# Performance work log

Hardware: AMD Instinct MI355X
Metric: run time of the kernel (lower is better)

The kernel has to match this reference:

```python
import jax, jax.numpy as jnp
import numpy as np
from jax.ops import segment_sum

N_NODE, N_EDGE, D_IN, D_HID, N_CLS = 50000, 800000, 64, 64, 40


def setup_inputs() -> dict:
    key = jax.random.key(0)
    k1, k2, k3, k4 = jax.random.split(key, 4)
    x = jax.random.normal(k1, (N_NODE, D_IN), dtype=jnp.float32)
    edge_index = jax.random.randint(k2, (2, N_EDGE), 0, N_NODE, dtype=jnp.int64)
    W1 = jax.random.normal(k3, (D_IN, D_HID), dtype=jnp.float32) * (1.0 / np.sqrt(D_IN))
    b1 = jnp.zeros((D_HID,), dtype=jnp.float32)
    W2 = jax.random.normal(k4, (D_HID, N_CLS), dtype=jnp.float32) * (1.0 / np.sqrt(D_HID))
    b2 = jnp.zeros((N_CLS,), dtype=jnp.float32)
    return {"x": x, "edge_index": edge_index, "W1": W1, "b1": b1, "W2": W2, "b2": b2}


def _att_weights(fea, row, col, n):
    # edge-parallel cosine similarity (sklearn cosine_similarity restricted to edges)
    nrm = jnp.sqrt(jnp.sum(fea * fea, axis=1, keepdims=True))
    fn = fea / jnp.maximum(nrm, 1e-12)
    sim = jnp.sum(fn[row] * fn[col], axis=1)                 # [E]
    sim = jnp.where(sim < 0.1, 0.0, sim)                      # threshold
    # L1 row-normalization (sim >= 0 after threshold)
    rs = segment_sum(sim, row, num_segments=n)                # [N]
    sim_n = jnp.where(sim > 0, sim / jnp.maximum(rs[row], 1e-12), 0.0)
    # degree-based self-loop weight lam = 1/(deg+1)
    deg = segment_sum((sim > 0).astype(fea.dtype), row, num_segments=n)
    lam = 1.0 / (deg + 1.0)
    # exp applied only to stored (nonzero) entries; zeroed edges stay 0
    w_edge = jnp.where(sim > 0, jnp.exp(sim_n), 0.0)          # [E]
    w_self = jnp.exp(lam)                                     # [N] self-loop weights
    return w_edge, w_self


def _gcn(h, W, b, row, col, w_edge, w_self, n):
    # symmetric-norm GCN over weighted edges + explicit self loops
    deg = segment_sum(w_edge, row, num_segments=n) + w_self
    dinv = 1.0 / jnp.sqrt(jnp.maximum(deg, 1e-12))
    h = h @ W                                                 # [N, F]
    coef = w_edge * dinv[row] * dinv[col]                     # [E]
    out = segment_sum(coef[:, None] * h[col], row, num_segments=n)
    out = out + (w_self * dinv * dinv)[:, None] * h + b
    return out


def reference(x, edge_index, W1, b1, W2, b2):
    n = x.shape[0]
    row, col = edge_index[0], edge_index[1]
    # layer 1: attention coefs from raw features
    w1e, w1s = _att_weights(x, row, col, n)
    h = jax.nn.relu(_gcn(x, W1, b1, row, col, w1e, w1s, n))
    # layer 2: attention coefs recomputed on hidden features (dropout = eval mode)
    w2e, w2s = _att_weights(h, row, col, n)
    out = _gcn(h, W2, b2, row, col, w2e, w2s, n)
    return jax.nn.log_softmax(out, axis=1)
```

## Files before the change

kernel.cpp:

```cpp
#include <hip/hip_runtime.h>
#include <math.h>


#define ATT_CAP 96
#define EPB     2048
#define RPB     128
#define NBUCK_MAX 512
#define CAPB    4096

__global__ void k_normfn(const float* __restrict__ fea, float* __restrict__ fn, int n)
{
    int gid  = blockIdx.x * blockDim.x + threadIdx.x;
    int wid  = gid >> 6;
    int lane = threadIdx.x & 63;
    if (wid >= n) return;
    float v = fea[(size_t)wid * 64 + lane];
    float s = v * v;
#pragma unroll
    for (int off = 32; off > 0; off >>= 1) s += __shfl_xor(s, off);
    float inv = 1.0f / fmaxf(sqrtf(s), 1e-12f);
    fn[(size_t)wid * 64 + lane] = v * inv;
}

__global__ void k_bhist(const int* __restrict__ row, int* __restrict__ hist,
                        int* __restrict__ btot, int E, int nblkA, int nbuck)
{
    __shared__ int lh[NBUCK_MAX];
    int b = blockIdx.x;
    int ebeg = b * EPB, eend = ebeg + EPB; if (eend > E) eend = E;
    for (int i = threadIdx.x; i < nbuck; i += blockDim.x) lh[i] = 0;
    __syncthreads();
    for (int e = ebeg + threadIdx.x; e < eend; e += blockDim.x)
        atomicAdd(&lh[row[e] >> 7], 1);
    __syncthreads();
    for (int i = threadIdx.x; i < nbuck; i += blockDim.x) {
        int c = lh[i];
        hist[(size_t)i * nblkA + b] = c;
        if (c) atomicAdd(btot + i, c);
    }
}

__global__ void k_bscan(const int* __restrict__ btot, int* __restrict__ bbase, int nbuck)
{
    int lane = threadIdx.x;
    int K = (nbuck + 63) / 64;
    int beg = lane * K;
    int s = 0;
    for (int i = 0; i < K; ++i) { int idx = beg + i; if (idx < nbuck) s += btot[idx]; }
    int incl = s;
#pragma unroll
    for (int off = 1; off < 64; off <<= 1) {
        int v = __shfl_up(incl, off);
        if (lane >= off) incl += v;
    }
    int run = incl - s;
    for (int i = 0; i < K; ++i) {
        int idx = beg + i;
        if (idx < nbuck) { bbase[idx] = run; run += btot[idx]; }
    }
    if (lane == 63) bbase[nbuck] = incl;
}

__global__ void k_mscan(int* __restrict__ hist, const int* __restrict__ bbase,
                        int nbuck, int nblkA)
{
    int wib  = threadIdx.x >> 6;
    int j    = blockIdx.x * 4 + wib;
    int lane = threadIdx.x & 63;
    if (j >= nbuck) return;
    int run = bbase[j];
    size_t base = (size_t)j * nblkA;
    for (int b0 = 0; b0 < nblkA; b0 += 64) {
        int b = b0 + lane;
        int v = (b < nblkA) ? hist[base + b] : 0;
        int incl = v;
#pragma unroll
        for (int off = 1; off < 64; off <<= 1) {
            int t = __shfl_up(incl, off);
            if (lane >= off) incl += t;
        }
        if (b < nblkA) hist[base + b] = run + (incl - v);
        run += __shfl(incl, 63);
    }
}

__global__ void k_bscat(const int* __restrict__ row, const int* __restrict__ col,
                        const int* __restrict__ hist, int* __restrict__ ebuf,
                        int E, int nblkA, int nbuck)
{
    __shared__ int lh[NBUCK_MAX];
    int b = blockIdx.x;
    int ebeg = b * EPB, eend = ebeg + EPB; if (eend > E) eend = E;
    for (int i = threadIdx.x; i < nbuck; i += blockDim.x)
        lh[i] = hist[(size_t)i * nblkA + b];
    __syncthreads();
    for (int e = ebeg + threadIdx.x; e < eend; e += blockDim.x) {
        int r = row[e];
        int j = r >> 7;
        int pos = atomicAdd(&lh[j], 1);
        ebuf[pos] = ((r & (RPB - 1)) << 16) | col[e];
    }
}

__global__ void k_csr(const int* __restrict__ ebuf, const int* __restrict__ bbase,
                      int* __restrict__ rptr, int* __restrict__ col_s, int N, int E)
{
    __shared__ int pk[CAPB];
    __shared__ int lcol[CAPB];
    __shared__ int lcnt[RPB], lexc[RPB], lcur[RPB];
    int j = blockIdx.x;
    int beg = bbase[j], end = bbase[j + 1];
    int m = end - beg; if (m > CAPB) m = CAPB;
    int tid = threadIdx.x;
    for (int i = tid; i < m; i += blockDim.x) pk[i] = ebuf[beg + i];
    if (tid < RPB) lcnt[tid] = 0;
    __syncthreads();
    for (int i = tid; i < m; i += blockDim.x) atomicAdd(&lcnt[pk[i] >> 16], 1);
    __syncthreads();
    if (tid < 64) {
        int a = lcnt[2 * tid], b2 = lcnt[2 * tid + 1];
        int s = a + b2;
        int incl = s;
#pragma unroll
        for (int off = 1; off < 64; off <<= 1) {
            int v = __shfl_up(incl, off);
            if (tid >= off) incl += v;
        }
        int base = incl - s;
        lexc[2 * tid] = base;     lexc[2 * tid + 1] = base + a;
        lcur[2 * tid] = base;     lcur[2 * tid + 1] = base + a;
    }
    __syncthreads();
    for (int i = tid; i < m; i += blockDim.x) {
        int v = pk[i];
        int p = atomicAdd(&lcur[v >> 16], 1);
        lcol[p] = v & 0xFFFF;
    }
    __syncthreads();
    for (int i = tid; i < m; i += blockDim.x) col_s[beg + i] = lcol[i];
    if (tid < RPB) {
        int r = j * RPB + tid;
        if (r < N) rptr[r] = beg + lexc[tid];
    }
    if (j == 0 && tid == 0) rptr[N] = E;
}

__global__ void k_att(const float* __restrict__ fn,
                      const int* __restrict__ rptr, const int* __restrict__ col_s,
                      int* __restrict__ col_live, float* __restrict__ w_live,
                      int* __restrict__ lend, float* __restrict__ dinv,
                      float* __restrict__ selfc, int n)
{
    __shared__ float ssim[4][ATT_CAP];
    __shared__ int   scol[4][ATT_CAP];
    int wib  = threadIdx.x >> 6;
    int wid  = blockIdx.x * 4 + wib;
    int lane = threadIdx.x & 63;
    if (wid >= n) return;
    int sub = lane & 7;
    int grp = lane >> 3;
    int beg = rptr[wid], end = rptr[wid + 1];
    int deg_all = end - beg;

    const float4* frp = (const float4*)(fn + (size_t)wid * 64);
    float4 a0 = frp[sub * 2], a1 = frp[sub * 2 + 1];

    float rs_part = 0.0f;
    int ngrp = (deg_all + 7) >> 3;
    for (int g = 0; g < ngrp; ++g) {
        int li = g * 8 + grp;
        float s = 0.0f; int c = 0;
        bool valid = (li < deg_all);
        if (valid) {
            c = col_s[beg + li];
            const float4* fcp = (const float4*)(fn + (size_t)c * 64);
            float4 b0 = fcp[sub * 2], b1 = fcp[sub * 2 + 1];
            float p = a0.x * b0.x + a0.y * b0.y + a0.z * b0.z + a0.w * b0.w
                    + a1.x * b1.x + a1.y * b1.y + a1.z * b1.z + a1.w * b1.w;
            p += __shfl_xor(p, 1);
            p += __shfl_xor(p, 2);
            p += __shfl_xor(p, 4);
            s = (p < 0.1f) ? 0.0f : p;
        }
        if (sub == 0 && valid) {
            if (li < ATT_CAP) { ssim[wib][li] = s; scol[wib][li] = c; }
            if (s > 0.0f) rs_part += s;
        }
    }
#pragma unroll
    for (int off = 32; off > 0; off >>= 1) rs_part += __shfl_xor(rs_part, off);
    float denom = fmaxf(rs_part, 1e-12f);

    int   nlive = 0;
    float sw_lane = 0.0f;
    for (int base = 0; base < deg_all; base += 64) {
        int li = base + lane;
        bool valid = (li < deg_all);
        float s = 0.0f; int c = 0;
        if (valid) {
            if (li < ATT_CAP) { s = ssim[wib][li]; c = scol[wib][li]; }
            else {
                c = col_s[beg + li];
                const float* fr = fn + (size_t)wid * 64;
                const float* fc = fn + (size_t)c * 64;
                float p = 0.0f;
                for (int k = 0; k < 64; ++k) p += fr[k] * fc[k];
                s = (p < 0.1f) ? 0.0f : p;
            }
        }
        float w = (valid && s > 0.0f) ? expf(s / denom) : 0.0f;
        unsigned long long M = __ballot(w > 0.0f);
        int rank = __popcll(M & ((1ull << lane) - 1ull));
        if (w > 0.0f) {
            col_live[beg + nlive + rank] = c;
            w_live[beg + nlive + rank]   = w;
            sw_lane += w;
        }
        nlive += __popcll(M);
    }
#pragma unroll
    for (int off = 32; off > 0; off >>= 1) sw_lane += __shfl_xor(sw_lane, off);

    if (lane == 0) {
        float wself = expf(1.0f / ((float)nlive + 1.0f));
        float D  = sw_lane + wself;
        float di = rsqrtf(fmaxf(D, 1e-12f));
        lend[wid]  = beg + nlive;
        dinv[wid]  = di;
        selfc[wid] = wself * di * di;
    }
}

template <int F, typename InT, typename OutT>
__global__ void k_gemm(const InT* __restrict__ fea, const float* __restrict__ W,
                       OutT* __restrict__ out, int n)
{
    constexpr int R = 256 / F;
    __shared__ float sW[64 * F];
    __shared__ float sX[R * 64];
    int tid = threadIdx.x;
    for (int i = tid; i < 64 * F; i += 256) sW[i] = W[i];
    int base = blockIdx.x * R;
    for (int i = tid; i < R * 64; i += 256) {
        int rr = base + i / 64;
        sX[i] = (rr < n) ? (float)fea[(size_t)rr * 64 + (i & 63)] : 0.0f;
    }
    __syncthreads();
    int rl = tid / F, j = tid % F;
    if (rl >= R) return;
    int r = base + rl;
    if (r >= n) return;
    float acc = 0.0f;
#pragma unroll
    for (int k = 0; k < 64; ++k) acc = fmaf(sX[rl * 64 + k], sW[k * F + j], acc);
    out[(size_t)r * F + j] = (OutT)acc;
}

template <int F>
__device__ inline float agg_core_live(const _Float16* __restrict__ h,
                                      const float* __restrict__ dinv,
                                      const int* __restrict__ col_live,
                                      const float* __restrict__ w_live,
                                      int beg, int lend_, int lane)
{
    float acc = 0.0f;
    bool active = (F == 64) ? true : (lane < F);
    for (int base = beg; base < lend_; base += 64) {
        int idx = base + lane;
        int cv = 0; float wv = 0.0f;
        if (idx < lend_) { cv = col_live[idx]; wv = w_live[idx]; }
        int cnt = lend_ - base; if (cnt > 64) cnt = 64;
        for (int j = 0; j < cnt; j += 4) {
            int   c0 = __shfl(cv, j);     float w0 = __shfl(wv, j);
            int   c1 = __shfl(cv, j + 1); float w1 = __shfl(wv, j + 1);
            int   c2 = __shfl(cv, j + 2); float w2 = __shfl(wv, j + 2);
            int   c3 = __shfl(cv, j + 3); float w3 = __shfl(wv, j + 3);
            float d0 = dinv[c0], d1 = dinv[c1], d2 = dinv[c2], d3 = dinv[c3];
            float h0 = 0.0f, h1 = 0.0f, h2 = 0.0f, h3 = 0.0f;
            if (active) {
                h0 = (float)h[(size_t)c0 * F + lane];
                h1 = (float)h[(size_t)c1 * F + lane];
                h2 = (float)h[(size_t)c2 * F + lane];
                h3 = (float)h[(size_t)c3 * F + lane];
            }
            acc += w0 * d0 * h0;
            acc += w1 * d1 * h1;
            acc += w2 * d2 * h2;
            acc += w3 * d3 * h3;
        }
    }
    return acc;
}

__global__ void k_agg64(const _Float16* __restrict__ h, const float* __restrict__ w_live,
                        const int* __restrict__ col_live,
                        const float* __restrict__ dinv, const float* __restrict__ selfc,
                        const float* __restrict__ b, const int* __restrict__ row_ptr,
                        const int* __restrict__ lend,
                        _Float16* __restrict__ hrelu16, float* __restrict__ fnh, int n)
{
    int gid  = blockIdx.x * blockDim.x + threadIdx.x;
    int wid  = gid >> 6;
    int lane = threadIdx.x & 63;
    if (wid >= n) return;
    int beg = row_ptr[wid], le = lend[wid];
    float acc = agg_core_live<64>(h, dinv, col_live, w_live, beg, le, lane);
    float hs  = (float)h[(size_t)wid * 64 + lane];
    float v = dinv[wid] * acc + selfc[wid] * hs + b[lane];
    v = fmaxf(v, 0.0f);
    hrelu16[(size_t)wid * 64 + lane] = (_Float16)v;
    float s = v * v;
#pragma unroll
    for (int off = 32; off > 0; off >>= 1) s += __shfl_xor(s, off);
    float inv = 1.0f / fmaxf(sqrtf(s), 1e-12f);
    fnh[(size_t)wid * 64 + lane] = v * inv;
}

__global__ void k_agg40_lsm(const _Float16* __restrict__ h2, const float* __restrict__ w_live,
                            const int* __restrict__ col_live,
                            const float* __restrict__ dinv, const float* __restrict__ selfc,
                            const float* __restrict__ b, const int* __restrict__ row_ptr,
                            const int* __restrict__ lend,
                            float* __restrict__ out, int n)
{
    constexpr int F = 40;
    int gid  = blockIdx.x * blockDim.x + threadIdx.x;
    int wid  = gid >> 6;
    int lane = threadIdx.x & 63;
    if (wid >= n) return;
    int beg = row_ptr[wid], le = lend[wid];
    float acc = agg_core_live<F>(h2, dinv, col_live, w_live, beg, le, lane);
    bool active = (lane < F);
    float v = 0.0f;
    if (active) {
        float hs = (float)h2[(size_t)wid * F + lane];
        v = dinv[wid] * acc + selfc[wid] * hs + b[lane];
    }
    float m = active ? v : -__builtin_inff();
#pragma unroll
    for (int off = 32; off > 0; off >>= 1) m = fmaxf(m, __shfl_xor(m, off));
    float ex = active ? expf(v - m) : 0.0f;
    float s = ex;
#pragma unroll
    for (int off = 32; off > 0; off >>= 1) s += __shfl_xor(s, off);
    if (active) out[(size_t)wid * F + lane] = v - m - logf(s);
}

extern "C" void kernel_launch(void* const* d_in, const int* in_sizes, int n_in,
                              void* d_out, int out_size, void* d_ws, size_t ws_size,
                              hipStream_t stream)
{
    const float* x  = (const float*)d_in[0];
    const int*   ei = (const int*)d_in[1];
    const float* W1 = (const float*)d_in[2];
    const float* b1 = (const float*)d_in[3];
    const float* W2 = (const float*)d_in[4];
    const float* b2 = (const float*)d_in[5];
    float* out = (float*)d_out;

    const int N = in_sizes[0] / 64;
    const int E = in_sizes[1] / 2;
    const int* row = ei;
    const int* col = ei + E;

    const int nblkA = (E + EPB - 1) / EPB;
    const int nbuck = (N + RPB - 1) / RPB;

    char* p = (char*)d_ws;
    auto alloc = [&](size_t bytes) -> char* {
        char* r = p; p += (bytes + 255) & ~(size_t)255; return r;
    };
    float*     fn     = (float*)alloc((size_t)N * 64 * 4);
    float*     dinv   = (float*)alloc((size_t)N * 4);
    float*     selfc  = (float*)alloc((size_t)N * 4);
    _Float16*  h1h    = (_Float16*)alloc((size_t)N * 64 * 2);
    _Float16*  hrelu  = (_Float16*)alloc((size_t)N * 64 * 2);
    _Float16*  h2h    = (_Float16*)alloc((size_t)N * 40 * 2);
    float*     fnh    = (float*)alloc((size_t)N * 64 * 4);
    int*       rptr   = (int*)alloc((size_t)(N + 1) * 4);
    int*       lendv  = (int*)alloc((size_t)N * 4);
    int*       col_s  = (int*)alloc((size_t)E * 4);
    int*       col_lv = (int*)alloc((size_t)E * 4);
    float*     w_lv   = (float*)alloc((size_t)E * 4);
    int*       ebuf   = (int*)alloc((size_t)E * 4);
    int*       hist   = (int*)alloc((size_t)nbuck * nblkA * 4);
    int*       btot   = (int*)alloc((size_t)nbuck * 4);
    int*       bbase  = (int*)alloc((size_t)(nbuck + 1) * 4);

    const int TB = 256;
    int blk_nodeWave = (N * 64 + TB - 1) / TB;
    int blk_node4    = (N + 3) / 4;

    hipMemsetAsync(btot, 0, (size_t)nbuck * 4, stream);

    k_bhist<<<nblkA, TB, 0, stream>>>(row, hist, btot, E, nblkA, nbuck);
    k_bscan<<<1, 64, 0, stream>>>(btot, bbase, nbuck);
    k_mscan<<<(nbuck + 3) / 4, TB, 0, stream>>>(hist, bbase, nbuck, nblkA);
    k_bscat<<<nblkA, TB, 0, stream>>>(row, col, hist, ebuf, E, nblkA, nbuck);
    k_csr<<<nbuck, TB, 0, stream>>>(ebuf, bbase, rptr, col_s, N, E);

    k_normfn<<<blk_nodeWave, TB, 0, stream>>>(x, fn, N);
    k_att<<<blk_node4, TB, 0, stream>>>(fn, rptr, col_s, col_lv, w_lv, lendv,
                                        dinv, selfc, N);
    k_gemm<64, float, _Float16><<<(N + 3) / 4, TB, 0, stream>>>(x, W1, h1h, N);
    k_agg64<<<blk_nodeWave, TB, 0, stream>>>(h1h, w_lv, col_lv, dinv, selfc, b1,
                                             rptr, lendv, hrelu, fnh, N);

    k_att<<<blk_node4, TB, 0, stream>>>(fnh, rptr, col_s, col_lv, w_lv, lendv,
                                        dinv, selfc, N);
    k_gemm<40, _Float16, _Float16><<<(N + 5) / 6, TB, 0, stream>>>(hrelu, W2, h2h, N);
    k_agg40_lsm<<<blk_nodeWave, TB, 0, stream>>>(h2h, w_lv, col_lv, dinv, selfc, b2,
                                                 rptr, lendv, out, N);
}
```

Baseline: 288.8 us.

## Prescale features by dinv, pack col/weight pairs, vectorize edge gather

Measured after the change: 285.5 us. About the same (-1.1%).

```diff
diff --git a/kernel.cpp b/kernel.cpp
--- a/kernel.cpp
+++ b/kernel.cpp
@@ -7,6 +7,8 @@
 #define RPB     128
 #define NBUCK_MAX 512
 #define CAPB    4096
+
+typedef _Float16 half4 __attribute__((ext_vector_type(4)));
 
 __global__ void k_normfn(const float* __restrict__ fea, float* __restrict__ fn, int n)
 {
@@ -147,9 +149,8 @@
 
 __global__ void k_att(const float* __restrict__ fn,
                       const int* __restrict__ rptr, const int* __restrict__ col_s,
-                      int* __restrict__ col_live, float* __restrict__ w_live,
-                      int* __restrict__ lend, float* __restrict__ dinv,
-                      float* __restrict__ selfc, int n)
+                      int2* __restrict__ cw, int* __restrict__ lend,
+                      float* __restrict__ dinv, float* __restrict__ selfc, int n)
 {
     __shared__ float ssim[4][ATT_CAP];
     __shared__ int   scol[4][ATT_CAP];
@@ -212,8 +213,8 @@
         unsigned long long M = __ballot(w > 0.0f);
         int rank = __popcll(M & ((1ull << lane) - 1ull));
         if (w > 0.0f) {
-            col_live[beg + nlive + rank] = c;
-            w_live[beg + nlive + rank]   = w;
+            int2 pw; pw.x = c; pw.y = __float_as_int(w);
+            cw[beg + nlive + rank] = pw;
             sw_lane += w;
         }
         nlive += __popcll(M);
@@ -227,13 +228,13 @@
         float di = rsqrtf(fmaxf(D, 1e-12f));
         lend[wid]  = beg + nlive;
         dinv[wid]  = di;
-        selfc[wid] = wself * di * di;
-    }
-}
-
-template <int F, typename InT, typename OutT>
+        selfc[wid] = wself * di;
+    }
+}
+
+template <int F, typename InT>
 __global__ void k_gemm(const InT* __restrict__ fea, const float* __restrict__ W,
-                       OutT* __restrict__ out, int n)
+                       const float* __restrict__ scale, _Float16* __restrict__ out, int n)
 {
     constexpr int R = 256 / F;
     __shared__ float sW[64 * F];
@@ -253,47 +254,49 @@
     float acc = 0.0f;
 #pragma unroll
     for (int k = 0; k < 64; ++k) acc = fmaf(sX[rl * 64 + k], sW[k * F + j], acc);
-    out[(size_t)r * F + j] = (OutT)acc;
+    out[(size_t)r * F + j] = (_Float16)(acc * scale[r]);
 }
 
 template <int F>
-__device__ inline float agg_core_live(const _Float16* __restrict__ h,
-                                      const float* __restrict__ dinv,
-                                      const int* __restrict__ col_live,
-                                      const float* __restrict__ w_live,
-                                      int beg, int lend_, int lane)
-{
-    float acc = 0.0f;
-    bool active = (F == 64) ? true : (lane < F);
+__device__ inline float agg_core_t(const _Float16* __restrict__ hd,
+                                   const int2* __restrict__ cw,
+                                   int beg, int lend_, int lane)
+{
+    int q  = lane & 15;
+    int eg = lane >> 4;
+    bool qact = (F == 64) ? true : (q < (F >> 2));
+    float acc0 = 0.f, acc1 = 0.f, acc2 = 0.f, acc3 = 0.f;
     for (int base = beg; base < lend_; base += 64) {
         int idx = base + lane;
         int cv = 0; float wv = 0.0f;
-        if (idx < lend_) { cv = col_live[idx]; wv = w_live[idx]; }
+        if (idx < lend_) { int2 pw = cw[idx]; cv = pw.x; wv = __int_as_float(pw.y); }
         int cnt = lend_ - base; if (cnt > 64) cnt = 64;
         for (int j = 0; j < cnt; j += 4) {
-            int   c0 = __shfl(cv, j);     float w0 = __shfl(wv, j);
-            int   c1 = __shfl(cv, j + 1); float w1 = __shfl(wv, j + 1);
-            int   c2 = __shfl(cv, j + 2); float w2 = __shfl(wv, j + 2);
-            int   c3 = __shfl(cv, j + 3); float w3 = __shfl(wv, j + 3);
-            float d0 = dinv[c0], d1 = dinv[c1], d2 = dinv[c2], d3 = dinv[c3];
-            float h0 = 0.0f, h1 = 0.0f, h2 = 0.0f, h3 = 0.0f;
-            if (active) {
-                h0 = (float)h[(size_t)c0 * F + lane];
-                h1 = (float)h[(size_t)c1 * F + lane];
-                h2 = (float)h[(size_t)c2 * F + lane];
-                h3 = (float)h[(size_t)c3 * F + lane];
+            int   c = __shfl(cv, j + eg);
+            float w = __shfl(wv, j + eg);
+            if (qact) {
+                half4 hv = *(const half4*)(hd + (size_t)c * F + q * 4);
+                acc0 += w * (float)hv.x;
+                acc1 += w * (float)hv.y;
+                acc2 += w * (float)hv.z;
+                acc3 += w * (float)hv.w;
             }
-            acc += w0 * d0 * h0;
-            acc += w1 * d1 * h1;
-            acc += w2 * d2 * h2;
-            acc += w3 * d3 * h3;
-        }
-    }
-    return acc;
-}
-
-__global__ void k_agg64(const _Float16* __restrict__ h, const float* __restrict__ w_live,
-                        const int* __restrict__ col_live,
+        }
+    }
+    acc0 += __shfl_xor(acc0, 16); acc0 += __shfl_xor(acc0, 32);
+    acc1 += __shfl_xor(acc1, 16); acc1 += __shfl_xor(acc1, 32);
+    acc2 += __shfl_xor(acc2, 16); acc2 += __shfl_xor(acc2, 32);
+    acc3 += __shfl_xor(acc3, 16); acc3 += __shfl_xor(acc3, 32);
+    int srcq = lane >> 2;
+    float a0 = __shfl(acc0, srcq);
+    float a1 = __shfl(acc1, srcq);
+    float a2 = __shfl(acc2, srcq);
+    float a3 = __shfl(acc3, srcq);
+    int k = lane & 3;
+    return (k == 0) ? a0 : (k == 1) ? a1 : (k == 2) ? a2 : a3;
+}
+
+__global__ void k_agg64(const _Float16* __restrict__ hd, const int2* __restrict__ cw,
                         const float* __restrict__ dinv, const float* __restrict__ selfc,
                         const float* __restrict__ b, const int* __restrict__ row_ptr,
                         const int* __restrict__ lend,
@@ -304,9 +307,9 @@
     int lane = threadIdx.x & 63;
     if (wid >= n) return;
     int beg = row_ptr[wid], le = lend[wid];
-    float acc = agg_core_live<64>(h, dinv, col_live, w_live, beg, le, lane);
-    float hs  = (float)h[(size_t)wid * 64 + lane];
-    float v = dinv[wid] * acc + selfc[wid] * hs + b[lane];
+    float accf = agg_core_t<64>(hd, cw, beg, le, lane);
+    float hs  = (float)hd[(size_t)wid * 64 + lane];
+    float v = dinv[wid] * accf + selfc[wid] * hs + b[lane];
     v = fmaxf(v, 0.0f);
     hrelu16[(size_t)wid * 64 + lane] = (_Float16)v;
     float s = v * v;
@@ -316,8 +319,7 @@
     fnh[(size_t)wid * 64 + lane] = v * inv;
 }
 
-__global__ void k_agg40_lsm(const _Float16* __restrict__ h2, const float* __restrict__ w_live,
-                            const int* __restrict__ col_live,
+__global__ void k_agg40_lsm(const _Float16* __restrict__ hd2, const int2* __restrict__ cw,
                             const float* __restrict__ dinv, const float* __restrict__ selfc,
                             const float* __restrict__ b, const int* __restrict__ row_ptr,
                             const int* __restrict__ lend,
@@ -329,12 +331,12 @@
     int lane = threadIdx.x & 63;
     if (wid >= n) return;
     int beg = row_ptr[wid], le = lend[wid];
-    float acc = agg_core_live<F>(h2, dinv, col_live, w_live, beg, le, lane);
+    float accf = agg_core_t<F>(hd2, cw, beg, le, lane);
     bool active = (lane < F);
     float v = 0.0f;
     if (active) {
-        float hs = (float)h2[(size_t)wid * F + lane];
-        v = dinv[wid] * acc + selfc[wid] * hs + b[lane];
+        float hs = (float)hd2[(size_t)wid * F + lane];
+        v = dinv[wid] * accf + selfc[wid] * hs + b[lane];
     }
     float m = active ? v : -__builtin_inff();
 #pragma unroll
@@ -373,15 +375,14 @@
     float*     fn     = (float*)alloc((size_t)N * 64 * 4);
     float*     dinv   = (float*)alloc((size_t)N * 4);
     float*     selfc  = (float*)alloc((size_t)N * 4);
-    _Float16*  h1h    = (_Float16*)alloc((size_t)N * 64 * 2);
+    _Float16*  hd1    = (_Float16*)alloc((size_t)N * 64 * 2);
     _Float16*  hrelu  = (_Float16*)alloc((size_t)N * 64 * 2);
-    _Float16*  h2h    = (_Float16*)alloc((size_t)N * 40 * 2);
+    _Float16*  hd2    = (_Float16*)alloc((size_t)N * 40 * 2);
     float*     fnh    = (float*)alloc((size_t)N * 64 * 4);
     int*       rptr   = (int*)alloc((size_t)(N + 1) * 4);
     int*       lendv  = (int*)alloc((size_t)N * 4);
     int*       col_s  = (int*)alloc((size_t)E * 4);
-    int*       col_lv = (int*)alloc((size_t)E * 4);
-    float*     w_lv   = (float*)alloc((size_t)E * 4);
+    int2*      cw     = (int2*)alloc((size_t)E * 8);
     int*       ebuf   = (int*)alloc((size_t)E * 4);
     int*       hist   = (int*)alloc((size_t)nbuck * nblkA * 4);
     int*       btot   = (int*)alloc((size_t)nbuck * 4);
@@ -400,15 +401,13 @@
     k_csr<<<nbuck, TB, 0, stream>>>(ebuf, bbase, rptr, col_s, N, E);
 
     k_normfn<<<blk_nodeWave, TB, 0, stream>>>(x, fn, N);
-    k_att<<<blk_node4, TB, 0, stream>>>(fn, rptr, col_s, col_lv, w_lv, lendv,
-                                        dinv, selfc, N);
-    k_gemm<64, float, _Float16><<<(N + 3) / 4, TB, 0, stream>>>(x, W1, h1h, N);
-    k_agg64<<<blk_nodeWave, TB, 0, stream>>>(h1h, w_lv, col_lv, dinv, selfc, b1,
+    k_att<<<blk_node4, TB, 0, stream>>>(fn, rptr, col_s, cw, lendv, dinv, selfc, N);
+    k_gemm<64, float><<<(N + 3) / 4, TB, 0, stream>>>(x, W1, dinv, hd1, N);
+    k_agg64<<<blk_nodeWave, TB, 0, stream>>>(hd1, cw, dinv, selfc, b1,
                                              rptr, lendv, hrelu, fnh, N);
 
-    k_att<<<blk_node4, TB, 0, stream>>>(fnh, rptr, col_s, col_lv, w_lv, lendv,
-                                        dinv, selfc, N);
-    k_gemm<40, _Float16, _Float16><<<(N + 5) / 6, TB, 0, stream>>>(hrelu, W2, h2h, N);
-    k_agg40_lsm<<<blk_nodeWave, TB, 0, stream>>>(h2h, w_lv, col_lv, dinv, selfc, b2,
+    k_att<<<blk_node4, TB, 0, stream>>>(fnh, rptr, col_s, cw, lendv, dinv, selfc, N);
+    k_gemm<40, _Float16><<<(N + 5) / 6, TB, 0, stream>>>(hrelu, W2, dinv, hd2, N);
+    k_agg40_lsm<<<blk_nodeWave, TB, 0, stream>>>(hd2, cw, dinv, selfc, b2,
                                                  rptr, lendv, out, N);
 }
```
